# Optimization experiments

Hardware: AMD Instinct MI355X
Metric: run time of the kernel (lower is better)

Reference implementation:

```python
import jax, jax.numpy as jnp
import numpy as np


def setup_inputs() -> dict:
    key = jax.random.key(0)
    k1, k2, k3, k4 = jax.random.split(key, 4)
    n, m = 4096, 1024  # n video frames, 1024-d features
    scale = 0.02
    return {
        "x": jax.random.normal(k1, (n, m), dtype=jnp.float32),
        "WQ": jax.random.normal(k2, (m, m), dtype=jnp.float32) * scale,  # torch Linear weight [out,in]
        "WK": jax.random.normal(k3, (m, m), dtype=jnp.float32) * scale,
        "WV": jax.random.normal(k4, (m, m), dtype=jnp.float32) * scale,
    }


def _quaternion_logits(q, k):
    """Hamilton-product attention logits: 4 tensors of shape [Lq, Lk]."""
    qr, qx, qy, qz = jnp.split(q, 4, axis=-1)
    kr, kx, ky, kz = jnp.split(k, 4, axis=-1)
    dot = lambda a, b: jnp.einsum('qd,kd->qk', a, b)
    r = dot(qr, kr) - dot(qx, kx) - dot(qy, ky) - dot(qz, kz)
    i = dot(qr, kx) + dot(qx, kr) + dot(qy, kz) - dot(qz, ky)
    j = dot(qr, ky) - dot(qx, kz) + dot(qy, kr) + dot(qz, kx)
    kk = dot(qr, kz) + dot(qx, ky) - dot(qy, kx) + dot(qz, kr)
    return [r, i, j, kk]


def reference(x, WQ, WK, WV):
    # QKV projections (torch Linear, no bias): y = x @ W.T
    Q = x @ WQ.T
    K = x @ WK.T
    V = x @ WV.T
    v_vals = jnp.split(V, 4, axis=-1)  # 4 chunks of depth d/4 (tensor2tensor quaternion attn)
    logits = _quaternion_logits(Q, K)
    outs = []
    w = None
    for l, v in zip(logits, v_vals):
        w = jax.nn.softmax(l, axis=-1)  # per-component softmax over keys
        outs.append(w @ v)
    y = jnp.concatenate(outs, axis=-1)  # [n, d]
    # original returns the attention weights from the last component (loop-leaked var)
    return y, w
```

## Files before the change

kernel.cpp:

```cpp
#include <hip/hip_runtime.h>
#include <cmath>

typedef __attribute__((ext_vector_type(8))) short short8;
typedef __attribute__((ext_vector_type(8))) unsigned short ushort8_t;
typedef __attribute__((ext_vector_type(8))) _Float16 half8;
typedef __attribute__((ext_vector_type(4))) float f32x4;
typedef unsigned short u16;

__device__ __forceinline__ u16 f2h(float f) {
    _Float16 h = (_Float16)f;
    return __builtin_bit_cast(u16, h);
}
__device__ __forceinline__ float h2f(u16 b) {
    return (float)__builtin_bit_cast(_Float16, b);
}

#define GLD16(g, l)                                                              \
    __builtin_amdgcn_global_load_lds(                                            \
        (const __attribute__((address_space(1))) unsigned int*)(g),              \
        (__attribute__((address_space(3))) unsigned int*)(l), 16, 0, 0)

#define MFMA_F16(a, b, c)                                                        \
    __builtin_amdgcn_mfma_f32_16x16x32_f16(                                      \
        __builtin_bit_cast(half8, (a)), __builtin_bit_cast(half8, (b)), (c), 0, 0, 0)
#define SBAR() asm volatile("s_barrier" ::: "memory")

__global__ __launch_bounds__(256) void to_h_all(
    const float* __restrict__ x, const float* __restrict__ WQ,
    const float* __restrict__ WK, const float* __restrict__ WV,
    u16* __restrict__ xh, u16* __restrict__ Wh)
{
    int bid = blockIdx.x;
    const float* src;
    u16* dst;
    int off;
    if (bid < 4096) { src = x; dst = xh; off = bid; }
    else {
        int j = bid - 4096;
        int wsel = j >> 10;
        off = j & 1023;
        src = wsel == 0 ? WQ : (wsel == 1 ? WK : WV);
        dst = Wh + (size_t)wsel * 1024 * 1024;
    }
    int idx = off * 256 + threadIdx.x;
    float4 v = reinterpret_cast<const float4*>(src)[idx];
    ushort4 h;
    h.x = f2h(v.x); h.y = f2h(v.y); h.z = f2h(v.z); h.w = f2h(v.w);
    reinterpret_cast<ushort4*>(dst)[idx] = h;
}

__global__ __launch_bounds__(512, 2) void logits8(
    const u16* __restrict__ A, const u16* __restrict__ B, const u16* __restrict__ Bneg,
    u16* __restrict__ Ch, float* __restrict__ pm, float* __restrict__ ps,
    int perm_packed, int sign_packed)
{
    constexpr int NT = 16;
    __shared__ u16 L[2][2][256 * 64];
    const int tid = threadIdx.x;
    const int l = tid & 63, w = tid >> 6;
    const int wr = w >> 2, wc = w & 3;
    const int lr = l & 15, lh = l >> 4;
    const int bid = (int)blockIdx.x;
    const int swz = (bid & 7) * 32 + (bid >> 3);
    const int row0 = (swz >> 4) * 256, col0 = (swz & 15) * 256;
    const int srow = l >> 3;
    const int scol = ((l & 7) ^ (l >> 3)) * 8;

    f32x4 acc[8][4] = {};

    auto stage = [&](int t) {
        int kA = t * 64;
        int ch = kA >> 8;
        int p = (perm_packed >> (2 * ch)) & 3;
        const u16* Bsrc = ((sign_packed >> ch) & 1) ? Bneg : B;
        int kB = (p << 8) + (kA & 255);
        int bf = t & 1;
        #pragma unroll
        for (int i = 0; i < 4; ++i) {
            int r0 = w * 32 + i * 8;
            GLD16(&A[(size_t)(row0 + r0 + srow) * 1024 + kA + scol], &L[bf][0][r0 * 64]);
        }
        #pragma unroll
        for (int i = 0; i < 4; ++i) {
            int r0 = w * 32 + i * 8;
            GLD16(&Bsrc[(size_t)(col0 + r0 + srow) * 1024 + kB + scol], &L[bf][1][r0 * 64]);
        }
    };
    auto readA = [&](int bf, int m, int kh) -> short8 {
        int row = wr * 128 + m * 16 + lr;
        int c = ((kh * 4 + lh) ^ (lr & 7)) * 8;
        return *reinterpret_cast<const short8*>(&L[bf][0][row * 64 + c]);
    };
    auto readB = [&](int bf, int n, int kh) -> short8 {
        int row = wc * 64 + n * 16 + lr;
        int c = ((kh * 4 + lh) ^ (lr & 7)) * 8;
        return *reinterpret_cast<const short8*>(&L[bf][1][row * 64 + c]);
    };

    stage(0);
    stage(1);
    asm volatile("s_waitcnt vmcnt(8)" ::: "memory");
    SBAR();

    #pragma unroll 2
    for (int t = 0; t < NT; ++t) {
        const int bf = t & 1;
        short8 am[4][2], bn[4][2];
        #pragma unroll
        for (int m = 0; m < 4; ++m) { am[m][0] = readA(bf, m, 0); am[m][1] = readA(bf, m, 1); }
        #pragma unroll
        for (int n = 0; n < 2; ++n) { bn[n][0] = readB(bf, n, 0); bn[n][1] = readB(bf, n, 1); }
        SBAR();
        __builtin_amdgcn_s_setprio(1);
        #pragma unroll
        for (int m = 0; m < 4; ++m)
            #pragma unroll
            for (int n = 0; n < 2; ++n) {
                acc[m][n] = MFMA_F16(am[m][0], bn[n][0], acc[m][n]);
                acc[m][n] = MFMA_F16(am[m][1], bn[n][1], acc[m][n]);
            }
        __builtin_amdgcn_s_setprio(0);
        SBAR();
        #pragma unroll
        for (int n = 2; n < 4; ++n) { bn[n][0] = readB(bf, n, 0); bn[n][1] = readB(bf, n, 1); }
        SBAR();
        __builtin_amdgcn_s_setprio(1);
        #pragma unroll
        for (int m = 0; m < 4; ++m)
            #pragma unroll
            for (int n = 2; n < 4; ++n) {
                acc[m][n] = MFMA_F16(am[m][0], bn[n][0], acc[m][n]);
                acc[m][n] = MFMA_F16(am[m][1], bn[n][1], acc[m][n]);
            }
        __builtin_amdgcn_s_setprio(0);
        SBAR();
        #pragma unroll
        for (int m = 0; m < 4; ++m) { am[m][0] = readA(bf, 4 + m, 0); am[m][1] = readA(bf, 4 + m, 1); }
        SBAR();
        __builtin_amdgcn_s_setprio(1);
        #pragma unroll
        for (int m = 0; m < 4; ++m)
            #pragma unroll
            for (int n = 2; n < 4; ++n) {
                acc[4 + m][n] = MFMA_F16(am[m][0], bn[n][0], acc[4 + m][n]);
                acc[4 + m][n] = MFMA_F16(am[m][1], bn[n][1], acc[4 + m][n]);
            }
        __builtin_amdgcn_s_setprio(0);
        SBAR();
        if (t + 2 < NT) stage(t + 2);
        SBAR();
        __builtin_amdgcn_s_setprio(1);
        #pragma unroll
        for (int m = 0; m < 4; ++m)
            #pragma unroll
            for (int n = 0; n < 2; ++n) {
                acc[4 + m][n] = MFMA_F16(am[m][0], bn[n][0], acc[4 + m][n]);
                acc[4 + m][n] = MFMA_F16(am[m][1], bn[n][1], acc[4 + m][n]);
            }
        __builtin_amdgcn_s_setprio(0);
        if (t + 2 < NT) { asm volatile("s_waitcnt vmcnt(8)" ::: "memory"); }
        else           { asm volatile("s_waitcnt vmcnt(0)" ::: "memory"); }
        SBAR();
    }

    const int tcol = (col0 >> 6) + wc;
    float* T = reinterpret_cast<float*>(&L[0][0][0]) + w * 1088;
    const int rq = l >> 2;
    const int cq = l & 3;
    #pragma unroll
    for (int m = 0; m < 8; ++m) {
        #pragma unroll
        for (int n = 0; n < 4; ++n)
            #pragma unroll
            for (int j = 0; j < 4; ++j)
                T[(lh * 4 + j) * 68 + n * 16 + lr] = acc[m][n][j];
        float vals[16];
        #pragma unroll
        for (int q = 0; q < 4; ++q) {
            f32x4 v4 = *reinterpret_cast<const f32x4*>(&T[rq * 68 + cq * 16 + q * 4]);
            vals[q * 4 + 0] = v4[0]; vals[q * 4 + 1] = v4[1];
            vals[q * 4 + 2] = v4[2]; vals[q * 4 + 3] = v4[3];
        }
        float mx = vals[0];
        #pragma unroll
        for (int c = 1; c < 16; ++c) mx = fmaxf(mx, vals[c]);
        mx = fmaxf(mx, __shfl_xor(mx, 1, 64));
        mx = fmaxf(mx, __shfl_xor(mx, 2, 64));
        float s = 0.f;
        #pragma unroll
        for (int c = 0; c < 16; ++c) s += expf(vals[c] - mx);
        s += __shfl_xor(s, 1, 64);
        s += __shfl_xor(s, 2, 64);
        int row = row0 + wr * 128 + m * 16 + rq;
        if (cq == 0) {
            pm[(size_t)row * 64 + tcol] = mx;
            ps[(size_t)row * 64 + tcol] = s;
        }
        ushort8_t d0, d1;
        #pragma unroll
        for (int c = 0; c < 8; ++c) d0[c] = f2h(vals[c] - mx);
        #pragma unroll
        for (int c = 0; c < 8; ++c) d1[c] = f2h(vals[c + 8] - mx);
        size_t go = (size_t)row * 4096 + col0 + wc * 64 + cq * 16;
        *reinterpret_cast<ushort8_t*>(&Ch[go]) = d0;
        *reinterpret_cast<ushort8_t*>(&Ch[go + 8]) = d1;
    }
}

__global__ __launch_bounds__(512, 2) void qkv8(
    const u16* __restrict__ A, const u16* __restrict__ B,
    u16* __restrict__ Qh, u16* __restrict__ Kh, u16* __restrict__ Khn,
    u16* __restrict__ Vt)
{
    constexpr int NT = 16;
    __shared__ u16 L[2][2][256 * 64];
    const int tid = threadIdx.x;
    const int l = tid & 63, w = tid >> 6;
    const int wr = w >> 2, wc = w & 3;
    const int lr = l & 15, lh = l >> 4;
    const int bid = (int)blockIdx.x;
    const int wgid = (bid & 7) * 24 + (bid >> 3);
    const int row0 = (wgid / 12) * 256, col0 = (wgid % 12) * 256;
    const int srow = l >> 3;
    const int scol = ((l & 7) ^ (l >> 3)) * 8;

    f32x4 acc[8][4] = {};

    auto stage = [&](int t) {
        int k0 = t * 64;
        int bf = t & 1;
        #pragma unroll
        for (int i = 0; i < 4; ++i) {
            int r0 = w * 32 + i * 8;
            GLD16(&A[(size_t)(row0 + r0 + srow) * 1024 + k0 + scol], &L[bf][0][r0 * 64]);
        }
        #pragma unroll
        for (int i = 0; i < 4; ++i) {
            int r0 = w * 32 + i * 8;
            GLD16(&B[(size_t)(col0 + r0 + srow) * 1024 + k0 + scol], &L[bf][1][r0 * 64]);
        }
    };
    auto readA = [&](int bf, int m, int kh) -> short8 {
        int row = wr * 128 + m * 16 + lr;
        int c = ((kh * 4 + lh) ^ (lr & 7)) * 8;
        return *reinterpret_cast<const short8*>(&L[bf][0][row * 64 + c]);
    };
    auto readB = [&](int bf, int n, int kh) -> short8 {
        int row = wc * 64 + n * 16 + lr;
        int c = ((kh * 4 + lh) ^ (lr & 7)) * 8;
        return *reinterpret_cast<const short8*>(&L[bf][1][row * 64 + c]);
    };

    stage(0);
    stage(1);
    asm volatile("s_waitcnt vmcnt(8)" ::: "memory");
    SBAR();

    #pragma unroll 2
    for (int t = 0; t < NT; ++t) {
        const int bf = t & 1;
        short8 am[4][2], bn[4][2];
        #pragma unroll
        for (int m = 0; m < 4; ++m) { am[m][0] = readA(bf, m, 0); am[m][1] = readA(bf, m, 1); }
        #pragma unroll
        for (int n = 0; n < 2; ++n) { bn[n][0] = readB(bf, n, 0); bn[n][1] = readB(bf, n, 1); }
        SBAR();
        __builtin_amdgcn_s_setprio(1);
        #pragma unroll
        for (int m = 0; m < 4; ++m)
            #pragma unroll
            for (int n = 0; n < 2; ++n) {
                acc[m][n] = MFMA_F16(am[m][0], bn[n][0], acc[m][n]);
                acc[m][n] = MFMA_F16(am[m][1], bn[n][1], acc[m][n]);
            }
        __builtin_amdgcn_s_setprio(0);
        SBAR();
        #pragma unroll
        for (int n = 2; n < 4; ++n) { bn[n][0] = readB(bf, n, 0); bn[n][1] = readB(bf, n, 1); }
        SBAR();
        __builtin_amdgcn_s_setprio(1);
        #pragma unroll
        for (int m = 0; m < 4; ++m)
            #pragma unroll
            for (int n = 2; n < 4; ++n) {
                acc[m][n] = MFMA_F16(am[m][0], bn[n][0], acc[m][n]);
                acc[m][n] = MFMA_F16(am[m][1], bn[n][1], acc[m][n]);
            }
        __builtin_amdgcn_s_setprio(0);
        SBAR();
        #pragma unroll
        for (int m = 0; m < 4; ++m) { am[m][0] = readA(bf, 4 + m, 0); am[m][1] = readA(bf, 4 + m, 1); }
        SBAR();
        __builtin_amdgcn_s_setprio(1);
        #pragma unroll
        for (int m = 0; m < 4; ++m)
            #pragma unroll
            for (int n = 2; n < 4; ++n) {
                acc[4 + m][n] = MFMA_F16(am[m][0], bn[n][0], acc[4 + m][n]);
                acc[4 + m][n] = MFMA_F16(am[m][1], bn[n][1], acc[4 + m][n]);
            }
        __builtin_amdgcn_s_setprio(0);
        SBAR();
        if (t + 2 < NT) stage(t + 2);
        SBAR();
        __builtin_amdgcn_s_setprio(1);
        #pragma unroll
        for (int m = 0; m < 4; ++m)
            #pragma unroll
            for (int n = 0; n < 2; ++n) {
                acc[4 + m][n] = MFMA_F16(am[m][0], bn[n][0], acc[4 + m][n]);
                acc[4 + m][n] = MFMA_F16(am[m][1], bn[n][1], acc[4 + m][n]);
            }
        __builtin_amdgcn_s_setprio(0);
        if (t + 2 < NT) { asm volatile("s_waitcnt vmcnt(8)" ::: "memory"); }
        else           { asm volatile("s_waitcnt vmcnt(0)" ::: "memory"); }
        SBAR();
    }

    const int mode = col0 >> 10;
    #pragma unroll
    for (int m = 0; m < 8; ++m)
        #pragma unroll
        for (int n = 0; n < 4; ++n) {
            int gr = row0 + wr * 128 + m * 16 + lh * 4;
            int gc = col0 + wc * 64 + n * 16 + lr;
            int gcl = gc & 1023;
            f32x4 v = acc[m][n];
            if (mode == 0) {
                #pragma unroll
                for (int j = 0; j < 4; ++j)
                    Qh[(size_t)(gr + j) * 1024 + gcl] = f2h(v[j]);
            } else if (mode == 1) {
                #pragma unroll
                for (int j = 0; j < 4; ++j) {
                    u16 h = f2h(v[j]);
                    size_t o = (size_t)(gr + j) * 1024 + gcl;
                    Kh[o] = h; Khn[o] = h ^ 0x8000;
                }
            } else {
                ushort4 o;
                o.x = f2h(v[0]); o.y = f2h(v[1]); o.z = f2h(v[2]); o.w = f2h(v[3]);
                *reinterpret_cast<ushort4*>(&Vt[(size_t)gcl * 4096 + gr]) = o;
            }
        }
}

template<bool WRITE_W>
__global__ __launch_bounds__(256) void pv_fused(
    const u16* __restrict__ Lh, float* __restrict__ Wout,
    const u16* __restrict__ Vt, const float* __restrict__ pm,
    const float* __restrict__ ps, u16* __restrict__ ypart, int c256)
{
    __shared__ u16 As[64 * 64];
    __shared__ u16 Bs[256 * 64];
    __shared__ float Red[64][4];
    __shared__ float Ms[64], Is[64];
    const int tid = threadIdx.x;
    const int l = tid & 63, w = tid >> 6;
    const int lr = l & 15, lh = l >> 4;
    const int kc = blockIdx.x;
    const int row0 = blockIdx.y * 64;
    const int kbase = kc * 512;
    const int srow = l >> 3, scol = ((l & 7) ^ (l >> 3)) * 8;

    {
        int row = tid & 63, part = tid >> 6;
        const float* pmr = &pm[(size_t)(row0 + row) * 64 + part * 16];
        const float* psr = &ps[(size_t)(row0 + row) * 64 + part * 16];
        float M = -INFINITY;
        #pragma unroll
        for (int i = 0; i < 16; ++i) M = fmaxf(M, pmr[i]);
        Red[row][part] = M;
        __syncthreads();
        float Mg = fmaxf(fmaxf(Red[row][0], Red[row][1]),
                         fmaxf(Red[row][2], Red[row][3]));
        float S = 0.f;
        #pragma unroll
        for (int i = 0; i < 16; ++i) S += psr[i] * expf(pmr[i] - Mg);
        __syncthreads();
        Red[row][part] = S;
        __syncthreads();
        if (tid < 64) {
            float Sg = Red[tid][0] + Red[tid][1] + Red[tid][2] + Red[tid][3];
            Ms[tid] = Mg;
            Is[tid] = 1.0f / Sg;
        }
        __syncthreads();
    }

    float Mr[4], Ir[4];
    #pragma unroll
    for (int i = 0; i < 4; ++i) { int r = (tid >> 4) + i * 16; Mr[i] = Ms[r]; Ir[i] = Is[r]; }

    f32x4 acc[4][4] = {};

    for (int kt = 0; kt < 8; ++kt) {
        const int tcol = kc * 8 + kt;
        __syncthreads();
        #pragma unroll
        for (int i = 0; i < 4; ++i) {
            int idx = tid + i * 256;
            int r = idx >> 4, s4 = idx & 15;
            float coff = pm[(size_t)(row0 + r) * 64 + tcol] - Mr[i];
            size_t ga = (size_t)(row0 + r) * 4096 + kbase + kt * 64 + s4 * 4;
            ushort4 dv = *reinterpret_cast<const ushort4*>(&Lh[ga]);
            float e0 = expf(h2f(dv.x) + coff) * Ir[i];
            float e1 = expf(h2f(dv.y) + coff) * Ir[i];
            float e2 = expf(h2f(dv.z) + coff) * Ir[i];
            float e3 = expf(h2f(dv.w) + coff) * Ir[i];
            if (WRITE_W)
                *reinterpret_cast<float4*>(&Wout[ga]) = make_float4(e0, e1, e2, e3);
            ushort4 h;
            h.x = f2h(e0); h.y = f2h(e1); h.z = f2h(e2); h.w = f2h(e3);
            int dst = ((s4 >> 1) ^ (r & 7)) * 8 + (s4 & 1) * 4;
            *reinterpret_cast<ushort4*>(&As[r * 64 + dst]) = h;
        }
        #pragma unroll
        for (int i = 0; i < 8; ++i) {
            int r0 = w * 64 + i * 8;
            GLD16(&Vt[(size_t)(c256 + r0 + srow) * 4096 + kbase + kt * 64 + scol],
                  &Bs[r0 * 64]);
        }
        __syncthreads();
        #pragma unroll
        for (int kh = 0; kh < 2; ++kh) {
            short8 af[4], bfv[4];
            #pragma unroll
            for (int m = 0; m < 4; ++m)
                af[m] = *reinterpret_cast<const short8*>(
                    &As[(m * 16 + lr) * 64 + ((kh * 4 + lh) ^ (lr & 7)) * 8]);
            #pragma unroll
            for (int n = 0; n < 4; ++n)
                bfv[n] = *reinterpret_cast<const short8*>(
                    &Bs[(w * 64 + n * 16 + lr) * 64 + ((kh * 4 + lh) ^ (lr & 7)) * 8]);
            #pragma unroll
            for (int m = 0; m < 4; ++m)
                #pragma unroll
                for (int n = 0; n < 4; ++n)
                    acc[m][n] = MFMA_F16(af[m], bfv[n], acc[m][n]);
        }
    }

    #pragma unroll
    for (int m = 0; m < 4; ++m)
        #pragma unroll
        for (int n = 0; n < 4; ++n) {
            int rr = m * 16 + lh * 4;
            int col = w * 64 + n * 16 + lr;
            #pragma unroll
            for (int j = 0; j < 4; ++j)
                ypart[((size_t)kc * 4096 + row0 + rr + j) * 256 + col] = f2h(acc[m][n][j]);
        }
}

__global__ __launch_bounds__(256) void reduce_y(const u16* __restrict__ ypart,
                                                float* __restrict__ y, int c256)
{
    int idx = blockIdx.x * 256 + threadIdx.x;
    int r = idx >> 6, c4 = (idx & 63) * 4;
    float s0 = 0.f, s1 = 0.f, s2 = 0.f, s3 = 0.f;
    #pragma unroll
    for (int kc = 0; kc < 8; ++kc) {
        ushort4 p = *reinterpret_cast<const ushort4*>(
            &ypart[((size_t)kc * 4096 + r) * 256 + c4]);
        s0 += h2f(p.x); s1 += h2f(p.y); s2 += h2f(p.z); s3 += h2f(p.w);
    }
    *reinterpret_cast<float4*>(&y[(size_t)r * 1024 + c256 + c4]) =
        make_float4(s0, s1, s2, s3);
}

extern "C" void kernel_launch(void* const* d_in, const int* in_sizes, int n_in,
                              void* d_out, int out_size, void* d_ws, size_t ws_size,
                              hipStream_t stream)
{
    const int n = 4096, d = 1024;
    const float* x  = (const float*)d_in[0];
    const float* WQ = (const float*)d_in[1];
    const float* WK = (const float*)d_in[2];
    const float* WV = (const float*)d_in[3];

    float* y = (float*)d_out;
    float* wout = y + (size_t)n * d;

    u16* Lh   = (u16*)d_ws;
    u16* xh   = Lh;
    u16* Wh   = Lh + (size_t)n * 1024;
    u16* Qh   = Lh + (size_t)n * 4096;
    u16* Kh   = Qh  + (size_t)n * 1024;
    u16* Khn  = Kh  + (size_t)n * 1024;
    u16* Vt   = Khn + (size_t)n * 1024;
    u16* ypart = Vt + (size_t)d * 4096;
    float* pm = (float*)(ypart + (size_t)8 * n * 256);
    float* ps = pm + (size_t)n * 64;

    to_h_all<<<7168, 256, 0, stream>>>(x, WQ, WK, WV, xh, Wh);

    qkv8<<<192, 512, 0, stream>>>(xh, Wh, Qh, Kh, Khn, Vt);

    const int permv[4] = {0xE4, 0xB1, 0x4E, 0x1B};
    const int signv[4] = {0x0E, 0x08, 0x02, 0x04};

    for (int c = 0; c < 4; ++c) {
        logits8<<<256, 512, 0, stream>>>(Qh, Kh, Khn, Lh, pm, ps, permv[c], signv[c]);
        if (c == 3)
            pv_fused<true><<<dim3(8, 64), 256, 0, stream>>>(Lh, wout, Vt, pm, ps, ypart, c * 256);
        else
            pv_fused<false><<<dim3(8, 64), 256, 0, stream>>>(Lh, wout, Vt, pm, ps, ypart, c * 256);
        reduce_y<<<1024, 256, 0, stream>>>(ypart, y, c * 256);
    }
}
```

Measured before the change: 350.4 us.

## Replace 256x256 pipelined GEMM kernels with simple 128x128 single-buffered template

The two hand-pipelined 256x256-tile, 512-thread GEMM kernels (QKV projection and quaternion logits) are replaced by one templated 128x128-tile, 256-thread kernel. It uses single-buffered LDS, plain __syncthreads, and no setprio interleaving. Grids grow from 192/256 blocks to 768/1024, which improves occupancy and load balance across the CUs. In exchange it loses double-buffered load/compute overlap and halves per-tile reuse, so each block does more global/LDS traffic per FLOP.

```diff
diff --git a/kernel.cpp b/kernel.cpp
--- a/kernel.cpp
+++ b/kernel.cpp
@@ -23,7 +23,6 @@
 #define MFMA_F16(a, b, c)                                                        \
     __builtin_amdgcn_mfma_f32_16x16x32_f16(                                      \
         __builtin_bit_cast(half8, (a)), __builtin_bit_cast(half8, (b)), (c), 0, 0, 0)
-#define SBAR() asm volatile("s_barrier" ::: "memory")
 
 __global__ __launch_bounds__(256) void to_h_all(
     const float* __restrict__ x, const float* __restrict__ WQ,
@@ -49,300 +48,142 @@
     reinterpret_cast<ushort4*>(dst)[idx] = h;
 }
 
-__global__ __launch_bounds__(512, 2) void logits8(
+template<int MODE, int NCOL>
+__global__ __launch_bounds__(256) void gemm128(
     const u16* __restrict__ A, const u16* __restrict__ B, const u16* __restrict__ Bneg,
-    u16* __restrict__ Ch, float* __restrict__ pm, float* __restrict__ ps,
+    u16* __restrict__ out0, float* __restrict__ pm, float* __restrict__ ps,
+    u16* __restrict__ Kh, u16* __restrict__ Khn, u16* __restrict__ Vt,
     int perm_packed, int sign_packed)
 {
-    constexpr int NT = 16;
-    __shared__ u16 L[2][2][256 * 64];
+    __shared__ u16 LA[128 * 64];
+    __shared__ u16 LB[128 * 64];
     const int tid = threadIdx.x;
     const int l = tid & 63, w = tid >> 6;
-    const int wr = w >> 2, wc = w & 3;
+    const int wr = w >> 1, wc = w & 1;
     const int lr = l & 15, lh = l >> 4;
     const int bid = (int)blockIdx.x;
-    const int swz = (bid & 7) * 32 + (bid >> 3);
-    const int row0 = (swz >> 4) * 256, col0 = (swz & 15) * 256;
+    const int q = (NCOL * 32) >> 3;
+    const int swz = (bid & 7) * q + (bid >> 3);
+    const int row0 = (swz / NCOL) * 128, col0 = (swz % NCOL) * 128;
     const int srow = l >> 3;
     const int scol = ((l & 7) ^ (l >> 3)) * 8;
 
-    f32x4 acc[8][4] = {};
-
-    auto stage = [&](int t) {
-        int kA = t * 64;
-        int ch = kA >> 8;
-        int p = (perm_packed >> (2 * ch)) & 3;
-        const u16* Bsrc = ((sign_packed >> ch) & 1) ? Bneg : B;
-        int kB = (p << 8) + (kA & 255);
-        int bf = t & 1;
+    f32x4 acc[4][4] = {};
+
+    for (int t = 0; t < 16; ++t) {
+        int kA = t * 64, kB;
+        const u16* Bsrc = B;
+        if (MODE == 0) {
+            int ch = kA >> 8;
+            int p = (perm_packed >> (2 * ch)) & 3;
+            if ((sign_packed >> ch) & 1) Bsrc = Bneg;
+            kB = (p << 8) + (kA & 255);
+        } else {
+            kB = kA;
+        }
+        __syncthreads();
         #pragma unroll
         for (int i = 0; i < 4; ++i) {
-            int r0 = w * 32 + i * 8;
-            GLD16(&A[(size_t)(row0 + r0 + srow) * 1024 + kA + scol], &L[bf][0][r0 * 64]);
+            int r0 = (w * 4 + i) * 8;
+            GLD16(&A[(size_t)(row0 + r0 + srow) * 1024 + kA + scol], &LA[r0 * 64]);
         }
         #pragma unroll
         for (int i = 0; i < 4; ++i) {
-            int r0 = w * 32 + i * 8;
-            GLD16(&Bsrc[(size_t)(col0 + r0 + srow) * 1024 + kB + scol], &L[bf][1][r0 * 64]);
-        }
-    };
-    auto readA = [&](int bf, int m, int kh) -> short8 {
-        int row = wr * 128 + m * 16 + lr;
-        int c = ((kh * 4 + lh) ^ (lr & 7)) * 8;
-        return *reinterpret_cast<const short8*>(&L[bf][0][row * 64 + c]);
-    };
-    auto readB = [&](int bf, int n, int kh) -> short8 {
-        int row = wc * 64 + n * 16 + lr;
-        int c = ((kh * 4 + lh) ^ (lr & 7)) * 8;
-        return *reinterpret_cast<const short8*>(&L[bf][1][row * 64 + c]);
-    };
-
-    stage(0);
-    stage(1);
-    asm volatile("s_waitcnt vmcnt(8)" ::: "memory");
-    SBAR();
-
-    #pragma unroll 2
-    for (int t = 0; t < NT; ++t) {
-        const int bf = t & 1;
-        short8 am[4][2], bn[4][2];
-        #pragma unroll
-        for (int m = 0; m < 4; ++m) { am[m][0] = readA(bf, m, 0); am[m][1] = readA(bf, m, 1); }
-        #pragma unroll
-        for (int n = 0; n < 2; ++n) { bn[n][0] = readB(bf, n, 0); bn[n][1] = readB(bf, n, 1); }
-        SBAR();
-        __builtin_amdgcn_s_setprio(1);
-        #pragma unroll
-        for (int m = 0; m < 4; ++m)
-            #pragma unroll
-            for (int n = 0; n < 2; ++n) {
-                acc[m][n] = MFMA_F16(am[m][0], bn[n][0], acc[m][n]);
-                acc[m][n] = MFMA_F16(am[m][1], bn[n][1], acc[m][n]);
-            }
-        __builtin_amdgcn_s_setprio(0);
-        SBAR();
-        #pragma unroll
-        for (int n = 2; n < 4; ++n) { bn[n][0] = readB(bf, n, 0); bn[n][1] = readB(bf, n, 1); }
-        SBAR();
-        __builtin_amdgcn_s_setprio(1);
-        #pragma unroll
-        for (int m = 0; m < 4; ++m)
-            #pragma unroll
-            for (int n = 2; n < 4; ++n) {
-                acc[m][n] = MFMA_F16(am[m][0], bn[n][0], acc[m][n]);
-                acc[m][n] = MFMA_F16(am[m][1], bn[n][1], acc[m][n]);
-            }
-        __builtin_amdgcn_s_setprio(0);
-        SBAR();
-        #pragma unroll
-        for (int m = 0; m < 4; ++m) { am[m][0] = readA(bf, 4 + m, 0); am[m][1] = readA(bf, 4 + m, 1); }
-        SBAR();
-        __builtin_amdgcn_s_setprio(1);
-        #pragma unroll
-        for (int m = 0; m < 4; ++m)
-            #pragma unroll
-            for (int n = 2; n < 4; ++n) {
-                acc[4 + m][n] = MFMA_F16(am[m][0], bn[n][0], acc[4 + m][n]);
-                acc[4 + m][n] = MFMA_F16(am[m][1], bn[n][1], acc[4 + m][n]);
-            }
-        __builtin_amdgcn_s_setprio(0);
-        SBAR();
-        if (t + 2 < NT) stage(t + 2);
-        SBAR();
-        __builtin_amdgcn_s_setprio(1);
-        #pragma unroll
-        for (int m = 0; m < 4; ++m)
-            #pragma unroll
-            for (int n = 0; n < 2; ++n) {
-                acc[4 + m][n] = MFMA_F16(am[m][0], bn[n][0], acc[4 + m][n]);
-                acc[4 + m][n] = MFMA_F16(am[m][1], bn[n][1], acc[4 + m][n]);
-            }
-        __builtin_amdgcn_s_setprio(0);
-        if (t + 2 < NT) { asm volatile("s_waitcnt vmcnt(8)" ::: "memory"); }
-        else           { asm volatile("s_waitcnt vmcnt(0)" ::: "memory"); }
-        SBAR();
-    }
-
-    const int tcol = (col0 >> 6) + wc;
-    float* T = reinterpret_cast<float*>(&L[0][0][0]) + w * 1088;
-    const int rq = l >> 2;
-    const int cq = l & 3;
-    #pragma unroll
-    for (int m = 0; m < 8; ++m) {
-        #pragma unroll
-        for (int n = 0; n < 4; ++n)
-            #pragma unroll
-            for (int j = 0; j < 4; ++j)
-                T[(lh * 4 + j) * 68 + n * 16 + lr] = acc[m][n][j];
-        float vals[16];
-        #pragma unroll
-        for (int q = 0; q < 4; ++q) {
-            f32x4 v4 = *reinterpret_cast<const f32x4*>(&T[rq * 68 + cq * 16 + q * 4]);
-            vals[q * 4 + 0] = v4[0]; vals[q * 4 + 1] = v4[1];
-            vals[q * 4 + 2] = v4[2]; vals[q * 4 + 3] = v4[3];
-        }
-        float mx = vals[0];
-        #pragma unroll
-        for (int c = 1; c < 16; ++c) mx = fmaxf(mx, vals[c]);
-        mx = fmaxf(mx, __shfl_xor(mx, 1, 64));
-        mx = fmaxf(mx, __shfl_xor(mx, 2, 64));
-        float s = 0.f;
-        #pragma unroll
-        for (int c = 0; c < 16; ++c) s += expf(vals[c] - mx);
-        s += __shfl_xor(s, 1, 64);
-        s += __shfl_xor(s, 2, 64);
-        int row = row0 + wr * 128 + m * 16 + rq;
-        if (cq == 0) {
-            pm[(size_t)row * 64 + tcol] = mx;
-            ps[(size_t)row * 64 + tcol] = s;
-        }
-        ushort8_t d0, d1;
-        #pragma unroll
-        for (int c = 0; c < 8; ++c) d0[c] = f2h(vals[c] - mx);
-        #pragma unroll
-        for (int c = 0; c < 8; ++c) d1[c] = f2h(vals[c + 8] - mx);
-        size_t go = (size_t)row * 4096 + col0 + wc * 64 + cq * 16;
-        *reinterpret_cast<ushort8_t*>(&Ch[go]) = d0;
-        *reinterpret_cast<ushort8_t*>(&Ch[go + 8]) = d1;
-    }
-}
-
-__global__ __launch_bounds__(512, 2) void qkv8(
-    const u16* __restrict__ A, const u16* __restrict__ B,
-    u16* __restrict__ Qh, u16* __restrict__ Kh, u16* __restrict__ Khn,
-    u16* __restrict__ Vt)
-{
-    constexpr int NT = 16;
-    __shared__ u16 L[2][2][256 * 64];
-    const int tid = threadIdx.x;
-    const int l = tid & 63, w = tid >> 6;
-    const int wr = w >> 2, wc = w & 3;
-    const int lr = l & 15, lh = l >> 4;
-    const int bid = (int)blockIdx.x;
-    const int wgid = (bid & 7) * 24 + (bid >> 3);
-    const int row0 = (wgid / 12) * 256, col0 = (wgid % 12) * 256;
-    const int srow = l >> 3;
-    const int scol = ((l & 7) ^ (l >> 3)) * 8;
-
-    f32x4 acc[8][4] = {};
-
-    auto stage = [&](int t) {
-        int k0 = t * 64;
-        int bf = t & 1;
-        #pragma unroll
-        for (int i = 0; i < 4; ++i) {
-            int r0 = w * 32 + i * 8;
-            GLD16(&A[(size_t)(row0 + r0 + srow) * 1024 + k0 + scol], &L[bf][0][r0 * 64]);
-        }
-        #pragma unroll
-        for (int i = 0; i < 4; ++i) {
-            int r0 = w * 32 + i * 8;
-            GLD16(&B[(size_t)(col0 + r0 + srow) * 1024 + k0 + scol], &L[bf][1][r0 * 64]);
-        }
-    };
-    auto readA = [&](int bf, int m, int kh) -> short8 {
-        int row = wr * 128 + m * 16 + lr;
-        int c = ((kh * 4 + lh) ^ (lr & 7)) * 8;
-        return *reinterpret_cast<const short8*>(&L[bf][0][row * 64 + c]);
-    };
-    auto readB = [&](int bf, int n, int kh) -> short8 {
-        int row = wc * 64 + n * 16 + lr;
-        int c = ((kh * 4 + lh) ^ (lr & 7)) * 8;
-        return *reinterpret_cast<const short8*>(&L[bf][1][row * 64 + c]);
-    };
-
-    stage(0);
-    stage(1);
-    asm volatile("s_waitcnt vmcnt(8)" ::: "memory");
-    SBAR();
-
-    #pragma unroll 2
-    for (int t = 0; t < NT; ++t) {
-        const int bf = t & 1;
-        short8 am[4][2], bn[4][2];
-        #pragma unroll
-        for (int m = 0; m < 4; ++m) { am[m][0] = readA(bf, m, 0); am[m][1] = readA(bf, m, 1); }
-        #pragma unroll
-        for (int n = 0; n < 2; ++n) { bn[n][0] = readB(bf, n, 0); bn[n][1] = readB(bf, n, 1); }
-        SBAR();
-        __builtin_amdgcn_s_setprio(1);
-        #pragma unroll
-        for (int m = 0; m < 4; ++m)
-            #pragma unroll
-            for (int n = 0; n < 2; ++n) {
-                acc[m][n] = MFMA_F16(am[m][0], bn[n][0], acc[m][n]);
-                acc[m][n] = MFMA_F16(am[m][1], bn[n][1], acc[m][n]);
-            }
-        __builtin_amdgcn_s_setprio(0);
-        SBAR();
-        #pragma unroll
-        for (int n = 2; n < 4; ++n) { bn[n][0] = readB(bf, n, 0); bn[n][1] = readB(bf, n, 1); }
-        SBAR();
-        __builtin_amdgcn_s_setprio(1);
-        #pragma unroll
-        for (int m = 0; m < 4; ++m)
-            #pragma unroll
-            for (int n = 2; n < 4; ++n) {
-                acc[m][n] = MFMA_F16(am[m][0], bn[n][0], acc[m][n]);
-                acc[m][n] = MFMA_F16(am[m][1], bn[n][1], acc[m][n]);
-            }
-        __builtin_amdgcn_s_setprio(0);
-        SBAR();
-        #pragma unroll
-        for (int m = 0; m < 4; ++m) { am[m][0] = readA(bf, 4 + m, 0); am[m][1] = readA(bf, 4 + m, 1); }
-        SBAR();
-        __builtin_amdgcn_s_setprio(1);
-        #pragma unroll
-        for (int m = 0; m < 4; ++m)
-            #pragma unroll
-            for (int n = 2; n < 4; ++n) {
-                acc[4 + m][n] = MFMA_F16(am[m][0], bn[n][0], acc[4 + m][n]);
-                acc[4 + m][n] = MFMA_F16(am[m][1], bn[n][1], acc[4 + m][n]);
-            }
-        __builtin_amdgcn_s_setprio(0);
-        SBAR();
-        if (t + 2 < NT) stage(t + 2);
-        SBAR();
-        __builtin_amdgcn_s_setprio(1);
-        #pragma unroll
-        for (int m = 0; m < 4; ++m)
-            #pragma unroll
-            for (int n = 0; n < 2; ++n) {
-                acc[4 + m][n] = MFMA_F16(am[m][0], bn[n][0], acc[4 + m][n]);
-                acc[4 + m][n] = MFMA_F16(am[m][1], bn[n][1], acc[4 + m][n]);
-            }
-        __builtin_amdgcn_s_setprio(0);
-        if (t + 2 < NT) { asm volatile("s_waitcnt vmcnt(8)" ::: "memory"); }
-        else           { asm volatile("s_waitcnt vmcnt(0)" ::: "memory"); }
-        SBAR();
-    }
-
-    const int mode = col0 >> 10;
-    #pragma unroll
-    for (int m = 0; m < 8; ++m)
-        #pragma unroll
-        for (int n = 0; n < 4; ++n) {
-            int gr = row0 + wr * 128 + m * 16 + lh * 4;
-            int gc = col0 + wc * 64 + n * 16 + lr;
-            int gcl = gc & 1023;
-            f32x4 v = acc[m][n];
-            if (mode == 0) {
+            int r0 = (w * 4 + i) * 8;
+            GLD16(&Bsrc[(size_t)(col0 + r0 + srow) * 1024 + kB + scol], &LB[r0 * 64]);
+        }
+        __syncthreads();
+        #pragma unroll
+        for (int kh = 0; kh < 2; ++kh) {
+            short8 af[4], bf[4];
+            #pragma unroll
+            for (int m = 0; m < 4; ++m)
+                af[m] = *reinterpret_cast<const short8*>(
+                    &LA[(wr * 64 + m * 16 + lr) * 64 + ((kh * 4 + lh) ^ (lr & 7)) * 8]);
+            #pragma unroll
+            for (int n = 0; n < 4; ++n)
+                bf[n] = *reinterpret_cast<const short8*>(
+                    &LB[(wc * 64 + n * 16 + lr) * 64 + ((kh * 4 + lh) ^ (lr & 7)) * 8]);
+            #pragma unroll
+            for (int m = 0; m < 4; ++m)
+                #pragma unroll
+                for (int n = 0; n < 4; ++n)
+                    acc[m][n] = MFMA_F16(af[m], bf[n], acc[m][n]);
+        }
+    }
+
+    if (MODE == 0) {
+        __syncthreads();
+        const int tcol = (col0 >> 6) + wc;
+        float* T = reinterpret_cast<float*>(&LA[0]) + w * 1088;
+        const int rq = l >> 2;
+        const int cq = l & 3;
+        #pragma unroll
+        for (int m = 0; m < 4; ++m) {
+            #pragma unroll
+            for (int n = 0; n < 4; ++n)
                 #pragma unroll
                 for (int j = 0; j < 4; ++j)
-                    Qh[(size_t)(gr + j) * 1024 + gcl] = f2h(v[j]);
-            } else if (mode == 1) {
-                #pragma unroll
-                for (int j = 0; j < 4; ++j) {
-                    u16 h = f2h(v[j]);
-                    size_t o = (size_t)(gr + j) * 1024 + gcl;
-                    Kh[o] = h; Khn[o] = h ^ 0x8000;
+                    T[(lh * 4 + j) * 68 + n * 16 + lr] = acc[m][n][j];
+            float vals[16];
+            #pragma unroll
+            for (int qq = 0; qq < 4; ++qq) {
+                f32x4 v4 = *reinterpret_cast<const f32x4*>(&T[rq * 68 + cq * 16 + qq * 4]);
+                vals[qq * 4 + 0] = v4[0]; vals[qq * 4 + 1] = v4[1];
+                vals[qq * 4 + 2] = v4[2]; vals[qq * 4 + 3] = v4[3];
+            }
+            float mx = vals[0];
+            #pragma unroll
+            for (int c = 1; c < 16; ++c) mx = fmaxf(mx, vals[c]);
+            mx = fmaxf(mx, __shfl_xor(mx, 1, 64));
+            mx = fmaxf(mx, __shfl_xor(mx, 2, 64));
+            float s = 0.f;
+            #pragma unroll
+            for (int c = 0; c < 16; ++c) s += expf(vals[c] - mx);
+            s += __shfl_xor(s, 1, 64);
+            s += __shfl_xor(s, 2, 64);
+            int row = row0 + wr * 64 + m * 16 + rq;
+            if (cq == 0) {
+                pm[(size_t)row * 64 + tcol] = mx;
+                ps[(size_t)row * 64 + tcol] = s;
+            }
+            ushort8_t d0, d1;
+            #pragma unroll
+            for (int c = 0; c < 8; ++c) d0[c] = f2h(vals[c] - mx);
+            #pragma unroll
+            for (int c = 0; c < 8; ++c) d1[c] = f2h(vals[c + 8] - mx);
+            size_t go = (size_t)row * 4096 + col0 + wc * 64 + cq * 16;
+            *reinterpret_cast<ushort8_t*>(&out0[go]) = d0;
+            *reinterpret_cast<ushort8_t*>(&out0[go + 8]) = d1;
+        }
+    } else {
+        const int mode = col0 >> 10;
+        #pragma unroll
+        for (int m = 0; m < 4; ++m)
+            #pragma unroll
+            for (int n = 0; n < 4; ++n) {
+                int gr = row0 + wr * 64 + m * 16 + lh * 4;
+                int gc = col0 + wc * 64 + n * 16 + lr;
+                int gcl = gc & 1023;
+                f32x4 v = acc[m][n];
+                if (mode == 0) {
+                    #pragma unroll
+                    for (int j = 0; j < 4; ++j)
+                        out0[(size_t)(gr + j) * 1024 + gcl] = f2h(v[j]);
+                } else if (mode == 1) {
+                    #pragma unroll
+                    for (int j = 0; j < 4; ++j) {
+                        u16 h = f2h(v[j]);
+                        size_t o = (size_t)(gr + j) * 1024 + gcl;
+                        Kh[o] = h; Khn[o] = h ^ 0x8000;
+                    }
+                } else {
+                    ushort4 o;
+                    o.x = f2h(v[0]); o.y = f2h(v[1]); o.z = f2h(v[2]); o.w = f2h(v[3]);
+                    *reinterpret_cast<ushort4*>(&Vt[(size_t)gcl * 4096 + gr]) = o;
                 }
-            } else {
-                ushort4 o;
-                o.x = f2h(v[0]); o.y = f2h(v[1]); o.z = f2h(v[2]); o.w = f2h(v[3]);
-                *reinterpret_cast<ushort4*>(&Vt[(size_t)gcl * 4096 + gr]) = o;
             }
-        }
+    }
 }
 
 template<bool WRITE_W>
@@ -495,13 +336,15 @@
 
     to_h_all<<<7168, 256, 0, stream>>>(x, WQ, WK, WV, xh, Wh);
 
-    qkv8<<<192, 512, 0, stream>>>(xh, Wh, Qh, Kh, Khn, Vt);
+    gemm128<1, 24><<<768, 256, 0, stream>>>(
+        xh, Wh, nullptr, Qh, nullptr, nullptr, Kh, Khn, Vt, 0, 0);
 
     const int permv[4] = {0xE4, 0xB1, 0x4E, 0x1B};
     const int signv[4] = {0x0E, 0x08, 0x02, 0x04};
 
     for (int c = 0; c < 4; ++c) {
-        logits8<<<256, 512, 0, stream>>>(Qh, Kh, Khn, Lh, pm, ps, permv[c], signv[c]);
+        gemm128<0, 32><<<1024, 256, 0, stream>>>(
+            Qh, Kh, Khn, Lh, pm, ps, nullptr, nullptr, nullptr, permv[c], signv[c]);
         if (c == 3)
             pv_fused<true><<<dim3(8, 64), 256, 0, stream>>>(Lh, wout, Vt, pm, ps, ypart, c * 256);
         else
```

Result: slower. 417.7 us (+19.2%).
